# Performance work log

Measured on AMD Instinct MI355X. Metric: run time of the kernel, lower is better.

The kernel has to match this reference:

```python
import jax, jax.numpy as jnp
import numpy as np

D_MODEL = 512
NUM_HEADS = 8
DEPTH = D_MODEL // NUM_HEADS
PROJ_DIM = 256
SEQ_LEN = 4096
BATCH = 8


def _glorot(key, shape):
    fan_in, fan_out = shape[-2], shape[-1]
    limit = np.sqrt(6.0 / (fan_in + fan_out))
    return jax.random.uniform(key, shape, jnp.float32, -limit, limit)


def setup_inputs() -> dict:
    key = jax.random.key(0)
    ks = jax.random.split(key, 8)
    x = jax.random.normal(ks[0], (BATCH, SEQ_LEN, D_MODEL), jnp.float32)
    wq = _glorot(ks[1], (D_MODEL, D_MODEL))
    wk = _glorot(ks[2], (D_MODEL, D_MODEL))
    wv = _glorot(ks[3], (D_MODEL, D_MODEL))
    E = _glorot(ks[4], (NUM_HEADS, SEQ_LEN, PROJ_DIM))
    F = _glorot(ks[5], (NUM_HEADS, SEQ_LEN, PROJ_DIM))
    w_out = _glorot(ks[6], (D_MODEL, D_MODEL))
    b_out = jnp.zeros((D_MODEL,), jnp.float32)
    return {"x": x, "wq": wq, "wk": wk, "wv": wv, "E": E, "F": F,
            "w_out": w_out, "b_out": b_out}


def reference(x, wq, wk, wv, E, F, w_out, b_out):
    b, n, _ = x.shape
    # QKV projections + split heads -> [b, h, n, d]
    def split_heads(t):
        return t.reshape(b, n, NUM_HEADS, DEPTH).transpose(0, 2, 1, 3)
    q = split_heads(x @ wq)
    k = split_heads(x @ wk)
    v = split_heads(x @ wv)
    # Linformer low-rank projection of K/V along sequence: [b,h,r,d]
    k_proj = jnp.einsum('bhnd,hnr->bhrd', k, E)
    v_proj = jnp.einsum('bhnd,hnr->bhrd', v, F)
    scale = 1.0 / jnp.sqrt(jnp.asarray(DEPTH, jnp.float32))
    scores = jnp.einsum('bhnd,bhrd->bhnr', q, k_proj) * scale  # [b,h,n,r]
    attn = jax.nn.softmax(scores, axis=-1)
    out = jnp.einsum('bhnr,bhrd->bhnd', attn, v_proj)
    out = out.transpose(0, 2, 1, 3).reshape(b, n, D_MODEL)
    return out @ w_out + b_out
```

## Files before the change

kernel.cpp:

```cpp
#include <hip/hip_runtime.h>

typedef unsigned short u16;
typedef unsigned int   u32;
typedef __bf16 bf16x8 __attribute__((ext_vector_type(8)));
typedef float  f32x4  __attribute__((ext_vector_type(4)));
typedef u16    u16x4  __attribute__((ext_vector_type(4)));

#define DEV __device__ __forceinline__

DEV u16 f2bf(float f) {
    u32 u = __builtin_bit_cast(u32, f);
    u = (u + 0x7fffu + ((u >> 16) & 1u)) >> 16;
    return (u16)u;
}

DEV void gload16(const void* g, void* l) {
    __builtin_amdgcn_global_load_lds((const __attribute__((address_space(1))) u32*)g,
                                     (__attribute__((address_space(3))) u32*)l, 16, 0, 0);
}

DEV void vmw(int n) {
    switch (n) {
        case 0:  asm volatile("s_waitcnt vmcnt(0)" ::: "memory"); break;
        case 4:  asm volatile("s_waitcnt vmcnt(4)" ::: "memory"); break;
        case 8:  asm volatile("s_waitcnt vmcnt(8)" ::: "memory"); break;
        default: asm volatile("s_waitcnt vmcnt(10)" ::: "memory"); break;
    }
}

__global__ __launch_bounds__(256) void k_prep(const float* __restrict__ x,
                                              const float* __restrict__ wq, const float* __restrict__ wk,
                                              const float* __restrict__ wv, const float* __restrict__ wo,
                                              const float* __restrict__ E, const float* __restrict__ F,
                                              u16* __restrict__ xb, u16* __restrict__ wcatT, u16* __restrict__ woT,
                                              u16* __restrict__ Et, u16* __restrict__ Ft) {
    __shared__ u16 tile[64][65];
    const int t = threadIdx.x;
    const int bid = blockIdx.x;
    if (bid < 16384) {
        int i = (bid * 256 + t) * 4;
        float4 v = *(const float4*)(x + i);
        u16x4 o;
        o[0] = f2bf(v.x); o[1] = f2bf(v.y); o[2] = f2bf(v.z); o[3] = f2bf(v.w);
        *(u16x4*)(xb + i) = o;
    } else if (bid < 20480) {
        const int b2 = bid - 16384;
        const int rt = b2 & 3, ntl = (b2 >> 2) & 63, h = (b2 >> 8) & 7, which = b2 >> 11;
        const float* src = (which ? F : E) + (size_t)h * 4096 * 256;
        u16* dst = (which ? Ft : Et) + (size_t)h * 256 * 4096;
        const int n0 = ntl * 64, r0 = rt * 64;
#pragma unroll
        for (int it = 0; it < 16; ++it) {
            const int idx = t + it * 256;
            const int nl = idx >> 6, rl = idx & 63;
            tile[nl][rl] = f2bf(src[(size_t)(n0 + nl) * 256 + r0 + rl]);
        }
        __syncthreads();
#pragma unroll
        for (int it = 0; it < 16; ++it) {
            const int idx = t + it * 256;
            const int rl = idx >> 6, nl = idx & 63;
            dst[(size_t)(r0 + rl) * 4096 + n0 + nl] = tile[nl][rl];
        }
    } else {
        const int b2 = bid - 20480;
        const int mi = b2 >> 6, tix = b2 & 63;
        const int jt = tix & 7, kt = tix >> 3;
        const float* w = (mi == 0) ? wq : (mi == 1) ? wk : (mi == 2) ? wv : wo;
        u16* dst = (mi < 3) ? (wcatT + mi * 262144) : woT;
#pragma unroll
        for (int it = 0; it < 16; ++it) {
            const int idx = t + it * 256;
            const int kl = idx >> 6, jl = idx & 63;
            tile[kl][jl] = f2bf(w[(kt * 64 + kl) * 512 + jt * 64 + jl]);
        }
        __syncthreads();
#pragma unroll
        for (int it = 0; it < 16; ++it) {
            const int idx = t + it * 256;
            const int jl = idx >> 6, kl = idx & 63;
            dst[(size_t)(jt * 64 + jl) * 512 + kt * 64 + kl] = tile[kl][jl];
        }
    }
}

template <int MODE>
__global__ __launch_bounds__(512, 2) void k_gemm8(const u16* __restrict__ A, const u16* __restrict__ Bm,
                                                  u16* __restrict__ Qo, u16* __restrict__ Kt, u16* __restrict__ Vt,
                                                  float* __restrict__ Of, const float* __restrict__ bias,
                                                  int M, int N, int K) {
    __shared__ __attribute__((aligned(16))) char smem[131072];
    const int tid = threadIdx.x;
    const int lane = tid & 63, w = tid >> 6;
    const int wr = w >> 2, wcn = w & 3;
    const int g = lane >> 4, l16 = lane & 15;
    const int nbm = M >> 8;
    const int bnc = N >> 8;
    const int bandw = nbm >> 3;
    const int bid = (int)blockIdx.x;
    const int xcd = bid & 7, loc = bid >> 3;
    const int bm = xcd * bandw + loc / bnc;
    const int bn = loc % bnc;
    const int m0 = bm << 8, n0 = bn << 8;
    const int NT = K >> 6;

    auto stage_h = [&](int h) {
        const int ktile = h >> 2, ty = h & 3;
        const int kh = ty >> 1;
        const int isB = ty & 1;
        const int slot = (ktile * 2 + kh) & 3;
        const u16* src = isB ? Bm : A;
        const int r0 = isB ? n0 : m0;
        char* base = smem + isB * 65536 + slot * 16384;
#pragma unroll
        for (int j = 0; j < 2; ++j) {
            const int off = j * 8192 + tid * 16;
            const int row = off >> 6, c = (off >> 4) & 3;
            const int sc = c ^ ((row >> 1) & 3);
            gload16(src + (size_t)(r0 + row) * K + ktile * 64 + kh * 32 + sc * 8, base + off);
        }
    };

    for (int h = 0; h < 6; ++h) stage_h(h);
    vmw(8);
    __builtin_amdgcn_sched_barrier(0);
    __builtin_amdgcn_s_barrier();

    f32x4 acc[8][4] = {};
    bf16x8 av[8];
    for (int kt = 0; kt < NT; ++kt) {
#pragma unroll
        for (int s = 0; s < 4; ++s) {
            const int kh = s >> 1, nh = s & 1;
            const int slot = (kt * 2 + kh) & 3;
            char* abase = smem + slot * 16384;
            char* bbase = smem + 65536 + slot * 16384;
            if (nh == 0) {
#pragma unroll
                for (int m = 0; m < 8; ++m) {
                    const int row = wr * 128 + m * 16 + l16;
                    const int c = g ^ ((row >> 1) & 3);
                    av[m] = *(const bf16x8*)(abase + row * 64 + c * 16);
                }
            }
            bf16x8 bv[2];
#pragma unroll
            for (int n = 0; n < 2; ++n) {
                const int col = wcn * 64 + nh * 32 + n * 16 + l16;
                const int c = g ^ ((col >> 1) & 3);
                bv[n] = *(const bf16x8*)(bbase + col * 64 + c * 16);
            }
            const int hst = kt * 4 + s + 6;
            if (hst < NT * 4) stage_h(hst);
            __builtin_amdgcn_s_setprio(1);
#pragma unroll
            for (int m = 0; m < 8; ++m)
#pragma unroll
                for (int n = 0; n < 2; ++n)
                    acc[m][nh * 2 + n] = __builtin_amdgcn_mfma_f32_16x16x32_bf16(av[m], bv[n], acc[m][nh * 2 + n], 0, 0, 0);
            __builtin_amdgcn_s_setprio(0);
            const bool last = (kt == NT - 1) && (s == 3);
            if (!last) {
                int n;
                if (s == 0)      n = (kt < NT - 1) ? 10 : 4;
                else if (s == 1) n = (kt < NT - 1) ? 8 : 0;
                else if (s == 2) n = (kt < NT - 2) ? 10 : ((kt == NT - 2) ? 8 : 0);
                else             n = (kt < NT - 2) ? 8 : 4;
                vmw(n);
                __builtin_amdgcn_sched_barrier(0);
                __builtin_amdgcn_s_barrier();
            }
        }
    }

    if (MODE == 0) {
        if (n0 < 512) {
#pragma unroll
            for (int m = 0; m < 8; ++m)
#pragma unroll
                for (int jn = 0; jn < 4; ++jn) {
                    const int col = n0 + wcn * 64 + jn * 16 + l16;
#pragma unroll
                    for (int i = 0; i < 4; ++i) {
                        const int row = m0 + wr * 128 + m * 16 + g * 4 + i;
                        Qo[(size_t)row * 512 + col] = f2bf(acc[m][jn][i]);
                    }
                }
        } else {
            u16* dst = (n0 < 1024) ? Kt : Vt;
#pragma unroll
            for (int m = 0; m < 8; ++m)
#pragma unroll
                for (int jn = 0; jn < 4; ++jn) {
                    const int col = (n0 + wcn * 64 + jn * 16 + l16) & 511;
                    const int h = col >> 6, d = col & 63;
                    const int rowb = m0 + wr * 128 + m * 16 + g * 4;
                    const int b = rowb >> 12, nn = rowb & 4095;
                    u16x4 pk;
#pragma unroll
                    for (int i = 0; i < 4; ++i) pk[i] = f2bf(acc[m][jn][i]);
                    *(u16x4*)(dst + ((size_t)((b * 8 + h) * 64 + d)) * 4096 + nn) = pk;
                }
        }
    } else {
#pragma unroll
        for (int m = 0; m < 8; ++m)
#pragma unroll
            for (int jn = 0; jn < 4; ++jn) {
                const int col = n0 + wcn * 64 + jn * 16 + l16;
                const float bb = bias[col];
#pragma unroll
                for (int i = 0; i < 4; ++i) {
                    const int row = m0 + wr * 128 + m * 16 + g * 4 + i;
                    Of[(size_t)row * N + col] = acc[m][jn][i] + bb;
                }
            }
    }
}

__global__ __launch_bounds__(256) void k_proj(const u16* __restrict__ Et, const u16* __restrict__ Ft,
                                              const u16* __restrict__ Kt, const u16* __restrict__ Vt,
                                              float* __restrict__ pbuf) {
    __shared__ __attribute__((aligned(16))) char smem[24576];
    const int tid = threadIdx.x;
    const int lane = tid & 63, wid = tid >> 6;
    const int wr = wid >> 1, wc = wid & 1;
    const int g = lane >> 4, l16 = lane & 15;
    const int bid = blockIdx.x;
    const int sp = bid >> 8, rest = bid & 255;
    const int mt = rest & 1, which = (rest >> 1) & 1, bh = rest >> 2;
    const int h = bh & 7;
    const u16* Ap = (which ? Ft : Et) + (size_t)h * 256 * 4096 + (size_t)mt * 128 * 4096;
    const u16* Bp = (which ? Vt : Kt) + (size_t)bh * 64 * 4096;

    f32x4 acc[4][2] = {};

    const int kbeg = sp * 1024;
    for (int k0 = kbeg; k0 < kbeg + 1024; k0 += 64) {
#pragma unroll
        for (int c = 0; c < 4; ++c) {
            const int off = c * 4096 + tid * 16;
            const int row = off >> 7;
            const int sc = ((off >> 4) & 7) ^ (row & 7);
            gload16(Ap + (size_t)row * 4096 + (k0 + sc * 8), smem + off);
            if (c < 2)
                gload16(Bp + (size_t)row * 4096 + (k0 + sc * 8), smem + 16384 + off);
        }
        __syncthreads();
#pragma unroll
        for (int kk = 0; kk < 64; kk += 32) {
            bf16x8 av[4], bv[2];
#pragma unroll
            for (int m = 0; m < 4; ++m) {
                const int r = wr * 64 + m * 16 + l16;
                av[m] = *(const bf16x8*)(smem + r * 128 + ((kk * 2 + g * 16) ^ ((r & 7) << 4)));
            }
#pragma unroll
            for (int n = 0; n < 2; ++n) {
                const int r = wc * 32 + n * 16 + l16;
                bv[n] = *(const bf16x8*)(smem + 16384 + r * 128 + ((kk * 2 + g * 16) ^ ((r & 7) << 4)));
            }
            __builtin_amdgcn_s_setprio(1);
#pragma unroll
            for (int m = 0; m < 4; ++m)
#pragma unroll
                for (int n = 0; n < 2; ++n)
                    acc[m][n] = __builtin_amdgcn_mfma_f32_16x16x32_bf16(av[m], bv[n], acc[m][n], 0, 0, 0);
            __builtin_amdgcn_s_setprio(0);
        }
        __syncthreads();
    }

    float* pb = pbuf + ((size_t)(sp * 2 + which) * 64 + bh) * 16384;
    if (which == 0) {
#pragma unroll
        for (int m = 0; m < 4; ++m)
#pragma unroll
            for (int n = 0; n < 2; ++n) {
                const int d = wc * 32 + n * 16 + l16;
#pragma unroll
                for (int i = 0; i < 4; ++i) {
                    const int rg = mt * 128 + wr * 64 + m * 16 + g * 4 + i;
                    pb[rg * 64 + d] = acc[m][n][i];
                }
            }
    } else {
#pragma unroll
        for (int m = 0; m < 4; ++m)
#pragma unroll
            for (int n = 0; n < 2; ++n) {
                const int d = wc * 32 + n * 16 + l16;
                const int r4 = mt * 128 + wr * 64 + m * 16 + g * 4;
                *(f32x4*)(pb + d * 256 + r4) = acc[m][n];
            }
    }
}

__global__ __launch_bounds__(256) void k_preduce(const float* __restrict__ pbuf, u16* __restrict__ outkv) {
    const int o = ((int)blockIdx.x * 256 + (int)threadIdx.x) * 4;
    f32x4 s = *(const f32x4*)(pbuf + o);
    s += *(const f32x4*)(pbuf + 2097152 + o);
    s += *(const f32x4*)(pbuf + 4194304 + o);
    s += *(const f32x4*)(pbuf + 6291456 + o);
    u16x4 r;
#pragma unroll
    for (int i = 0; i < 4; ++i) r[i] = f2bf(s[i]);
    *(u16x4*)(outkv + o) = r;
}

__global__ __launch_bounds__(256) void k_flash(const u16* __restrict__ Q, const u16* __restrict__ kp,
                                               const u16* __restrict__ vpT, u16* __restrict__ ctx) {
    __shared__ __attribute__((aligned(16))) char smem[65536];
    const int tid = threadIdx.x;
    const int lane = tid & 63, w = tid >> 6;
    const int g = lane >> 4, l16 = lane & 15;
    const int bid = blockIdx.x;
    const int nt = bid & 63, bh = bid >> 6;
    const int b = bh >> 3, h = bh & 7;
    const int n0 = nt * 64;

#pragma unroll
    for (int c = 0; c < 8; ++c) {
        const int off = c * 4096 + tid * 16;
        {
            const int row = off >> 7;
            const int sc = ((off >> 4) & 7) ^ (row & 7);
            gload16(kp + (size_t)bh * 16384 + row * 64 + sc * 8, smem + off);
        }
        {
            const int row = off >> 9;
            const int sc = ((off >> 4) & 31) ^ (row & 7);
            gload16(vpT + (size_t)bh * 16384 + row * 256 + sc * 8, smem + 32768 + off);
        }
    }
    const size_t qbase = (size_t)(b * 4096 + n0 + w * 16 + l16) * 512 + h * 64 + g * 8;
    bf16x8 qf0 = *(const bf16x8*)(Q + qbase);
    bf16x8 qf1 = *(const bf16x8*)(Q + qbase + 32);
    __syncthreads();

    f32x4 s[16];
    __builtin_amdgcn_s_setprio(1);
#pragma unroll
    for (int rt = 0; rt < 16; ++rt) {
        const int r = rt * 16 + l16;
        const int sw = (r & 7) << 4;
        bf16x8 kv0 = *(const bf16x8*)(smem + r * 128 + ((g * 16) ^ sw));
        bf16x8 kv1 = *(const bf16x8*)(smem + r * 128 + ((64 + g * 16) ^ sw));
        f32x4 z = {0.f, 0.f, 0.f, 0.f};
        z = __builtin_amdgcn_mfma_f32_16x16x32_bf16(qf0, kv0, z, 0, 0, 0);
        z = __builtin_amdgcn_mfma_f32_16x16x32_bf16(qf1, kv1, z, 0, 0, 0);
        s[rt] = z;
    }
    __builtin_amdgcn_s_setprio(0);

    float mx[4] = {-1e30f, -1e30f, -1e30f, -1e30f};
#pragma unroll
    for (int rt = 0; rt < 16; ++rt)
#pragma unroll
        for (int i = 0; i < 4; ++i) {
            s[rt][i] *= 0.125f;
            mx[i] = fmaxf(mx[i], s[rt][i]);
        }
#pragma unroll
    for (int i = 0; i < 4; ++i) {
        mx[i] = fmaxf(mx[i], __shfl_xor(mx[i], 1));
        mx[i] = fmaxf(mx[i], __shfl_xor(mx[i], 2));
        mx[i] = fmaxf(mx[i], __shfl_xor(mx[i], 4));
        mx[i] = fmaxf(mx[i], __shfl_xor(mx[i], 8));
    }
    float sm[4] = {0.f, 0.f, 0.f, 0.f};
#pragma unroll
    for (int rt = 0; rt < 16; ++rt)
#pragma unroll
        for (int i = 0; i < 4; ++i) {
            float e = __expf(s[rt][i] - mx[i]);
            s[rt][i] = e;
            sm[i] += e;
        }
#pragma unroll
    for (int i = 0; i < 4; ++i) {
        sm[i] += __shfl_xor(sm[i], 1);
        sm[i] += __shfl_xor(sm[i], 2);
        sm[i] += __shfl_xor(sm[i], 4);
        sm[i] += __shfl_xor(sm[i], 8);
    }

    __syncthreads();

#pragma unroll
    for (int rt = 0; rt < 16; ++rt)
#pragma unroll
        for (int i = 0; i < 4; ++i) {
            const int nrow = g * 4 + i;
            const int byte = w * 8192 + nrow * 512 + ((rt * 32 + l16 * 2) ^ ((nrow & 7) << 4));
            *(u16*)(smem + byte) = f2bf(s[rt][i]);
        }
    bf16x8 af[8];
#pragma unroll
    for (int ks = 0; ks < 8; ++ks) {
        const int byte = w * 8192 + l16 * 512 + ((ks * 64 + g * 16) ^ ((l16 & 7) << 4));
        af[ks] = *(const bf16x8*)(smem + byte);
    }
    f32x4 o[4] = {};
    __builtin_amdgcn_s_setprio(1);
#pragma unroll
    for (int dt = 0; dt < 4; ++dt)
#pragma unroll
        for (int ks = 0; ks < 8; ++ks) {
            const int row = dt * 16 + l16;
            const int byte = 32768 + row * 512 + ((ks * 64 + g * 16) ^ ((row & 7) << 4));
            bf16x8 bv = *(const bf16x8*)(smem + byte);
            o[dt] = __builtin_amdgcn_mfma_f32_16x16x32_bf16(af[ks], bv, o[dt], 0, 0, 0);
        }
    __builtin_amdgcn_s_setprio(0);
    float rinv[4];
#pragma unroll
    for (int i = 0; i < 4; ++i) rinv[i] = 1.0f / sm[i];
#pragma unroll
    for (int dt = 0; dt < 4; ++dt)
#pragma unroll
        for (int i = 0; i < 4; ++i) {
            const int row = b * 4096 + n0 + w * 16 + g * 4 + i;
            const int col = h * 64 + dt * 16 + l16;
            ctx[(size_t)row * 512 + col] = f2bf(o[dt][i] * rinv[i]);
        }
}


extern "C" void kernel_launch(void* const* d_in, const int* in_sizes, int n_in,
                              void* d_out, int out_size, void* d_ws, size_t ws_size,
                              hipStream_t stream) {
    const float* x  = (const float*)d_in[0];
    const float* wq = (const float*)d_in[1];
    const float* wk = (const float*)d_in[2];
    const float* wv = (const float*)d_in[3];
    const float* E  = (const float*)d_in[4];
    const float* F  = (const float*)d_in[5];
    const float* wo = (const float*)d_in[6];
    const float* bo = (const float*)d_in[7];
    float* out = (float*)d_out;
    u16* ws = (u16*)d_ws;

    u16* xb    = ws;
    u16* Qm    = ws + 16777216;
    u16* Kt    = ws + 33554432;
    u16* Vt    = ws + 50331648;
    u16* Et    = ws + 67108864;
    u16* Ft    = ws + 75497472;
    u16* wcatT = ws + 83886080;
    u16* woT   = ws + 84672512;
    u16* kpB   = ws + 84934656;
    u16* vpT   = ws + 85983232;
    float* pbuf = (float*)xb;
    u16* ctx   = xb;

    k_prep<<<20736, 256, 0, stream>>>(x, wq, wk, wv, wo, E, F, xb, wcatT, woT, Et, Ft);
    k_gemm8<0><<<768, 512, 0, stream>>>(xb, wcatT, Qm, Kt, Vt, nullptr, nullptr, 32768, 1536, 512);
    k_proj<<<1024, 256, 0, stream>>>(Et, Ft, Kt, Vt, pbuf);
    k_preduce<<<2048, 256, 0, stream>>>(pbuf, kpB);
    k_flash<<<4096, 256, 0, stream>>>(Qm, kpB, vpT, ctx);
    k_gemm8<1><<<256, 512, 0, stream>>>(ctx, woT, nullptr, nullptr, nullptr, out, bo, 32768, 512, 512);
}
```

Baseline: 368.2 us.

## Vectorize prep transposes, simplify GEMM pipeline, and reuse K/V tiles across query blocks

The prep kernel now reads float4 and writes u16x4 when transposing weights and E/F, with padded tiles. The GEMM main loop stages A and B half-k tiles together and runs a simpler loop of 32 MFMAs per step with its own waitcnt schedule. The attention kernel now runs 512 threads per block and loops over four 128-row query chunks, so each block loads the projected K/V tile into shared memory once for 512 query rows instead of 64. The trade-off is far fewer blocks, 128KB of LDS per block, and serial per-chunk work inside each block.

```diff
diff --git a/kernel.cpp b/kernel.cpp
--- a/kernel.cpp
+++ b/kernel.cpp
@@ -23,8 +23,7 @@
     switch (n) {
         case 0:  asm volatile("s_waitcnt vmcnt(0)" ::: "memory"); break;
         case 4:  asm volatile("s_waitcnt vmcnt(4)" ::: "memory"); break;
-        case 8:  asm volatile("s_waitcnt vmcnt(8)" ::: "memory"); break;
-        default: asm volatile("s_waitcnt vmcnt(10)" ::: "memory"); break;
+        default: asm volatile("s_waitcnt vmcnt(8)" ::: "memory"); break;
     }
 }
 
@@ -34,7 +33,7 @@
                                               const float* __restrict__ E, const float* __restrict__ F,
                                               u16* __restrict__ xb, u16* __restrict__ wcatT, u16* __restrict__ woT,
                                               u16* __restrict__ Et, u16* __restrict__ Ft) {
-    __shared__ u16 tile[64][65];
+    __shared__ u16 tile[64][68];
     const int t = threadIdx.x;
     const int bid = blockIdx.x;
     if (bid < 16384) {
@@ -50,17 +49,22 @@
         u16* dst = (which ? Ft : Et) + (size_t)h * 256 * 4096;
         const int n0 = ntl * 64, r0 = rt * 64;
 #pragma unroll
-        for (int it = 0; it < 16; ++it) {
+        for (int it = 0; it < 4; ++it) {
             const int idx = t + it * 256;
-            const int nl = idx >> 6, rl = idx & 63;
-            tile[nl][rl] = f2bf(src[(size_t)(n0 + nl) * 256 + r0 + rl]);
+            const int nl = idx >> 4, rq = (idx & 15) * 4;
+            float4 v = *(const float4*)(src + (size_t)(n0 + nl) * 256 + r0 + rq);
+            tile[rq + 0][nl] = f2bf(v.x);
+            tile[rq + 1][nl] = f2bf(v.y);
+            tile[rq + 2][nl] = f2bf(v.z);
+            tile[rq + 3][nl] = f2bf(v.w);
         }
         __syncthreads();
 #pragma unroll
-        for (int it = 0; it < 16; ++it) {
+        for (int it = 0; it < 4; ++it) {
             const int idx = t + it * 256;
-            const int rl = idx >> 6, nl = idx & 63;
-            dst[(size_t)(r0 + rl) * 4096 + n0 + nl] = tile[nl][rl];
+            const int rl = idx >> 4, nq = (idx & 15) * 4;
+            u16x4 vv = *(const u16x4*)&tile[rl][nq];
+            *(u16x4*)(dst + (size_t)(r0 + rl) * 4096 + n0 + nq) = vv;
         }
     } else {
         const int b2 = bid - 20480;
@@ -69,17 +73,22 @@
         const float* w = (mi == 0) ? wq : (mi == 1) ? wk : (mi == 2) ? wv : wo;
         u16* dst = (mi < 3) ? (wcatT + mi * 262144) : woT;
 #pragma unroll
-        for (int it = 0; it < 16; ++it) {
+        for (int it = 0; it < 4; ++it) {
             const int idx = t + it * 256;
-            const int kl = idx >> 6, jl = idx & 63;
-            tile[kl][jl] = f2bf(w[(kt * 64 + kl) * 512 + jt * 64 + jl]);
+            const int kl = idx >> 4, jq = (idx & 15) * 4;
+            float4 v = *(const float4*)(w + (size_t)(kt * 64 + kl) * 512 + jt * 64 + jq);
+            tile[jq + 0][kl] = f2bf(v.x);
+            tile[jq + 1][kl] = f2bf(v.y);
+            tile[jq + 2][kl] = f2bf(v.z);
+            tile[jq + 3][kl] = f2bf(v.w);
         }
         __syncthreads();
 #pragma unroll
-        for (int it = 0; it < 16; ++it) {
+        for (int it = 0; it < 4; ++it) {
             const int idx = t + it * 256;
-            const int jl = idx >> 6, kl = idx & 63;
-            dst[(size_t)(jt * 64 + jl) * 512 + kt * 64 + kl] = tile[kl][jl];
+            const int jl = idx >> 4, kq = (idx & 15) * 4;
+            u16x4 vv = *(const u16x4*)&tile[jl][kq];
+            *(u16x4*)(dst + (size_t)(jt * 64 + jl) * 512 + kt * 64 + kq) = vv;
         }
     }
 }
@@ -102,74 +111,61 @@
     const int bm = xcd * bandw + loc / bnc;
     const int bn = loc % bnc;
     const int m0 = bm << 8, n0 = bn << 8;
-    const int NT = K >> 6;
-
-    auto stage_h = [&](int h) {
-        const int ktile = h >> 2, ty = h & 3;
-        const int kh = ty >> 1;
-        const int isB = ty & 1;
-        const int slot = (ktile * 2 + kh) & 3;
-        const u16* src = isB ? Bm : A;
-        const int r0 = isB ? n0 : m0;
-        char* base = smem + isB * 65536 + slot * 16384;
-#pragma unroll
-        for (int j = 0; j < 2; ++j) {
-            const int off = j * 8192 + tid * 16;
-            const int row = off >> 6, c = (off >> 4) & 3;
-            const int sc = c ^ ((row >> 1) & 3);
-            gload16(src + (size_t)(r0 + row) * K + ktile * 64 + kh * 32 + sc * 8, base + off);
+    const int NP = K >> 5;
+
+    auto stage_pair = [&](int P) {
+        const int kt = P >> 1, kh = P & 1;
+        const int slot = P & 3;
+#pragma unroll
+        for (int isB = 0; isB < 2; ++isB) {
+            const u16* src = isB ? Bm : A;
+            const int r0 = isB ? n0 : m0;
+            char* base = smem + isB * 65536 + slot * 16384;
+#pragma unroll
+            for (int j = 0; j < 2; ++j) {
+                const int off = j * 8192 + tid * 16;
+                const int row = off >> 6, c = (off >> 4) & 3;
+                const int sc = c ^ ((row >> 1) & 3);
+                gload16(src + (size_t)(r0 + row) * K + kt * 64 + kh * 32 + sc * 8, base + off);
+            }
         }
     };
 
-    for (int h = 0; h < 6; ++h) stage_h(h);
+    stage_pair(0); stage_pair(1); stage_pair(2);
     vmw(8);
     __builtin_amdgcn_sched_barrier(0);
     __builtin_amdgcn_s_barrier();
 
     f32x4 acc[8][4] = {};
-    bf16x8 av[8];
-    for (int kt = 0; kt < NT; ++kt) {
-#pragma unroll
-        for (int s = 0; s < 4; ++s) {
-            const int kh = s >> 1, nh = s & 1;
-            const int slot = (kt * 2 + kh) & 3;
-            char* abase = smem + slot * 16384;
-            char* bbase = smem + 65536 + slot * 16384;
-            if (nh == 0) {
-#pragma unroll
-                for (int m = 0; m < 8; ++m) {
-                    const int row = wr * 128 + m * 16 + l16;
-                    const int c = g ^ ((row >> 1) & 3);
-                    av[m] = *(const bf16x8*)(abase + row * 64 + c * 16);
-                }
-            }
-            bf16x8 bv[2];
-#pragma unroll
-            for (int n = 0; n < 2; ++n) {
-                const int col = wcn * 64 + nh * 32 + n * 16 + l16;
-                const int c = g ^ ((col >> 1) & 3);
-                bv[n] = *(const bf16x8*)(bbase + col * 64 + c * 16);
-            }
-            const int hst = kt * 4 + s + 6;
-            if (hst < NT * 4) stage_h(hst);
-            __builtin_amdgcn_s_setprio(1);
-#pragma unroll
-            for (int m = 0; m < 8; ++m)
-#pragma unroll
-                for (int n = 0; n < 2; ++n)
-                    acc[m][nh * 2 + n] = __builtin_amdgcn_mfma_f32_16x16x32_bf16(av[m], bv[n], acc[m][nh * 2 + n], 0, 0, 0);
-            __builtin_amdgcn_s_setprio(0);
-            const bool last = (kt == NT - 1) && (s == 3);
-            if (!last) {
-                int n;
-                if (s == 0)      n = (kt < NT - 1) ? 10 : 4;
-                else if (s == 1) n = (kt < NT - 1) ? 8 : 0;
-                else if (s == 2) n = (kt < NT - 2) ? 10 : ((kt == NT - 2) ? 8 : 0);
-                else             n = (kt < NT - 2) ? 8 : 4;
-                vmw(n);
-                __builtin_amdgcn_sched_barrier(0);
-                __builtin_amdgcn_s_barrier();
-            }
+    for (int P = 0; P < NP; ++P) {
+        const int slot = P & 3;
+        char* abase = smem + slot * 16384;
+        char* bbase = smem + 65536 + slot * 16384;
+        bf16x8 av[8], bv[4];
+#pragma unroll
+        for (int m = 0; m < 8; ++m) {
+            const int row = wr * 128 + m * 16 + l16;
+            const int c = g ^ ((row >> 1) & 3);
+            av[m] = *(const bf16x8*)(abase + row * 64 + c * 16);
+        }
+#pragma unroll
+        for (int n = 0; n < 4; ++n) {
+            const int col = wcn * 64 + n * 16 + l16;
+            const int c = g ^ ((col >> 1) & 3);
+            bv[n] = *(const bf16x8*)(bbase + col * 64 + c * 16);
+        }
+        if (P + 3 < NP) stage_pair(P + 3);
+        __builtin_amdgcn_s_setprio(1);
+#pragma unroll
+        for (int m = 0; m < 8; ++m)
+#pragma unroll
+            for (int n = 0; n < 4; ++n)
+                acc[m][n] = __builtin_amdgcn_mfma_f32_16x16x32_bf16(av[m], bv[n], acc[m][n], 0, 0, 0);
+        __builtin_amdgcn_s_setprio(0);
+        if (P < NP - 1) {
+            vmw(P < NP - 3 ? 8 : (P == NP - 3 ? 4 : 0));
+            __builtin_amdgcn_sched_barrier(0);
+            __builtin_amdgcn_s_barrier();
         }
     }
 
@@ -308,20 +304,20 @@
     *(u16x4*)(outkv + o) = r;
 }
 
-__global__ __launch_bounds__(256) void k_flash(const u16* __restrict__ Q, const u16* __restrict__ kp,
+__global__ __launch_bounds__(512) void k_flash(const u16* __restrict__ Q, const u16* __restrict__ kp,
                                                const u16* __restrict__ vpT, u16* __restrict__ ctx) {
-    __shared__ __attribute__((aligned(16))) char smem[65536];
+    __shared__ __attribute__((aligned(16))) char smem[131072];
     const int tid = threadIdx.x;
     const int lane = tid & 63, w = tid >> 6;
     const int g = lane >> 4, l16 = lane & 15;
     const int bid = blockIdx.x;
-    const int nt = bid & 63, bh = bid >> 6;
+    const int seg = bid & 7, bh = bid >> 3;
     const int b = bh >> 3, h = bh & 7;
-    const int n0 = nt * 64;
-
-#pragma unroll
-    for (int c = 0; c < 8; ++c) {
-        const int off = c * 4096 + tid * 16;
+    const int n0 = seg * 512;
+
+#pragma unroll
+    for (int c = 0; c < 4; ++c) {
+        const int off = c * 8192 + tid * 16;
         {
             const int row = off >> 7;
             const int sc = ((off >> 4) & 7) ^ (row & 7);
@@ -333,97 +329,104 @@
             gload16(vpT + (size_t)bh * 16384 + row * 256 + sc * 8, smem + 32768 + off);
         }
     }
-    const size_t qbase = (size_t)(b * 4096 + n0 + w * 16 + l16) * 512 + h * 64 + g * 8;
-    bf16x8 qf0 = *(const bf16x8*)(Q + qbase);
-    bf16x8 qf1 = *(const bf16x8*)(Q + qbase + 32);
+    const size_t qrow0 = (size_t)(b * 4096 + n0 + w * 16 + l16) * 512 + h * 64 + g * 8;
+    bf16x8 qf0 = *(const bf16x8*)(Q + qrow0);
+    bf16x8 qf1 = *(const bf16x8*)(Q + qrow0 + 32);
     __syncthreads();
 
-    f32x4 s[16];
-    __builtin_amdgcn_s_setprio(1);
-#pragma unroll
-    for (int rt = 0; rt < 16; ++rt) {
-        const int r = rt * 16 + l16;
-        const int sw = (r & 7) << 4;
-        bf16x8 kv0 = *(const bf16x8*)(smem + r * 128 + ((g * 16) ^ sw));
-        bf16x8 kv1 = *(const bf16x8*)(smem + r * 128 + ((64 + g * 16) ^ sw));
-        f32x4 z = {0.f, 0.f, 0.f, 0.f};
-        z = __builtin_amdgcn_mfma_f32_16x16x32_bf16(qf0, kv0, z, 0, 0, 0);
-        z = __builtin_amdgcn_mfma_f32_16x16x32_bf16(qf1, kv1, z, 0, 0, 0);
-        s[rt] = z;
-    }
-    __builtin_amdgcn_s_setprio(0);
-
-    float mx[4] = {-1e30f, -1e30f, -1e30f, -1e30f};
-#pragma unroll
-    for (int rt = 0; rt < 16; ++rt)
+    const int pbase = 65536 + w * 8192;
+    for (int qp = 0; qp < 4; ++qp) {
+        f32x4 s[16];
+        __builtin_amdgcn_s_setprio(1);
+#pragma unroll
+        for (int rt = 0; rt < 16; ++rt) {
+            const int r = rt * 16 + l16;
+            const int sw = (r & 7) << 4;
+            bf16x8 kv0 = *(const bf16x8*)(smem + r * 128 + ((g * 16) ^ sw));
+            bf16x8 kv1 = *(const bf16x8*)(smem + r * 128 + ((64 + g * 16) ^ sw));
+            f32x4 z = {0.f, 0.f, 0.f, 0.f};
+            z = __builtin_amdgcn_mfma_f32_16x16x32_bf16(qf0, kv0, z, 0, 0, 0);
+            z = __builtin_amdgcn_mfma_f32_16x16x32_bf16(qf1, kv1, z, 0, 0, 0);
+            s[rt] = z;
+        }
+        __builtin_amdgcn_s_setprio(0);
+
+        if (qp < 3) {
+            const size_t qn = qrow0 + (size_t)(qp + 1) * 128 * 512;
+            qf0 = *(const bf16x8*)(Q + qn);
+            qf1 = *(const bf16x8*)(Q + qn + 32);
+        }
+
+        float mx[4] = {-1e30f, -1e30f, -1e30f, -1e30f};
+#pragma unroll
+        for (int rt = 0; rt < 16; ++rt)
+#pragma unroll
+            for (int i = 0; i < 4; ++i) {
+                s[rt][i] *= 0.125f;
+                mx[i] = fmaxf(mx[i], s[rt][i]);
+            }
 #pragma unroll
         for (int i = 0; i < 4; ++i) {
-            s[rt][i] *= 0.125f;
-            mx[i] = fmaxf(mx[i], s[rt][i]);
-        }
-#pragma unroll
-    for (int i = 0; i < 4; ++i) {
-        mx[i] = fmaxf(mx[i], __shfl_xor(mx[i], 1));
-        mx[i] = fmaxf(mx[i], __shfl_xor(mx[i], 2));
-        mx[i] = fmaxf(mx[i], __shfl_xor(mx[i], 4));
-        mx[i] = fmaxf(mx[i], __shfl_xor(mx[i], 8));
-    }
-    float sm[4] = {0.f, 0.f, 0.f, 0.f};
-#pragma unroll
-    for (int rt = 0; rt < 16; ++rt)
+            mx[i] = fmaxf(mx[i], __shfl_xor(mx[i], 1));
+            mx[i] = fmaxf(mx[i], __shfl_xor(mx[i], 2));
+            mx[i] = fmaxf(mx[i], __shfl_xor(mx[i], 4));
+            mx[i] = fmaxf(mx[i], __shfl_xor(mx[i], 8));
+        }
+        float sm[4] = {0.f, 0.f, 0.f, 0.f};
+#pragma unroll
+        for (int rt = 0; rt < 16; ++rt)
+#pragma unroll
+            for (int i = 0; i < 4; ++i) {
+                float e = __expf(s[rt][i] - mx[i]);
+                s[rt][i] = e;
+                sm[i] += e;
+            }
 #pragma unroll
         for (int i = 0; i < 4; ++i) {
-            float e = __expf(s[rt][i] - mx[i]);
-            s[rt][i] = e;
-            sm[i] += e;
-        }
-#pragma unroll
-    for (int i = 0; i < 4; ++i) {
-        sm[i] += __shfl_xor(sm[i], 1);
-        sm[i] += __shfl_xor(sm[i], 2);
-        sm[i] += __shfl_xor(sm[i], 4);
-        sm[i] += __shfl_xor(sm[i], 8);
-    }
-
-    __syncthreads();
-
-#pragma unroll
-    for (int rt = 0; rt < 16; ++rt)
-#pragma unroll
-        for (int i = 0; i < 4; ++i) {
-            const int nrow = g * 4 + i;
-            const int byte = w * 8192 + nrow * 512 + ((rt * 32 + l16 * 2) ^ ((nrow & 7) << 4));
-            *(u16*)(smem + byte) = f2bf(s[rt][i]);
-        }
-    bf16x8 af[8];
-#pragma unroll
-    for (int ks = 0; ks < 8; ++ks) {
-        const int byte = w * 8192 + l16 * 512 + ((ks * 64 + g * 16) ^ ((l16 & 7) << 4));
-        af[ks] = *(const bf16x8*)(smem + byte);
-    }
-    f32x4 o[4] = {};
-    __builtin_amdgcn_s_setprio(1);
-#pragma unroll
-    for (int dt = 0; dt < 4; ++dt)
+            sm[i] += __shfl_xor(sm[i], 1);
+            sm[i] += __shfl_xor(sm[i], 2);
+            sm[i] += __shfl_xor(sm[i], 4);
+            sm[i] += __shfl_xor(sm[i], 8);
+        }
+
+#pragma unroll
+        for (int rt = 0; rt < 16; ++rt)
+#pragma unroll
+            for (int i = 0; i < 4; ++i) {
+                const int nrow = g * 4 + i;
+                const int byte = pbase + nrow * 512 + ((rt * 32 + l16 * 2) ^ ((nrow & 7) << 4));
+                *(u16*)(smem + byte) = f2bf(s[rt][i]);
+            }
+        bf16x8 af[8];
 #pragma unroll
         for (int ks = 0; ks < 8; ++ks) {
-            const int row = dt * 16 + l16;
-            const int byte = 32768 + row * 512 + ((ks * 64 + g * 16) ^ ((row & 7) << 4));
-            bf16x8 bv = *(const bf16x8*)(smem + byte);
-            o[dt] = __builtin_amdgcn_mfma_f32_16x16x32_bf16(af[ks], bv, o[dt], 0, 0, 0);
-        }
-    __builtin_amdgcn_s_setprio(0);
-    float rinv[4];
-#pragma unroll
-    for (int i = 0; i < 4; ++i) rinv[i] = 1.0f / sm[i];
-#pragma unroll
-    for (int dt = 0; dt < 4; ++dt)
-#pragma unroll
-        for (int i = 0; i < 4; ++i) {
-            const int row = b * 4096 + n0 + w * 16 + g * 4 + i;
-            const int col = h * 64 + dt * 16 + l16;
-            ctx[(size_t)row * 512 + col] = f2bf(o[dt][i] * rinv[i]);
-        }
+            const int byte = pbase + l16 * 512 + ((ks * 64 + g * 16) ^ ((l16 & 7) << 4));
+            af[ks] = *(const bf16x8*)(smem + byte);
+        }
+        f32x4 o[4] = {};
+        __builtin_amdgcn_s_setprio(1);
+#pragma unroll
+        for (int dt = 0; dt < 4; ++dt)
+#pragma unroll
+            for (int ks = 0; ks < 8; ++ks) {
+                const int row = dt * 16 + l16;
+                const int byte = 32768 + row * 512 + ((ks * 64 + g * 16) ^ ((row & 7) << 4));
+                bf16x8 bv = *(const bf16x8*)(smem + byte);
+                o[dt] = __builtin_amdgcn_mfma_f32_16x16x32_bf16(af[ks], bv, o[dt], 0, 0, 0);
+            }
+        __builtin_amdgcn_s_setprio(0);
+        float rinv[4];
+#pragma unroll
+        for (int i = 0; i < 4; ++i) rinv[i] = 1.0f / sm[i];
+#pragma unroll
+        for (int dt = 0; dt < 4; ++dt)
+#pragma unroll
+            for (int i = 0; i < 4; ++i) {
+                const int row = b * 4096 + n0 + qp * 128 + w * 16 + g * 4 + i;
+                const int col = h * 64 + dt * 16 + l16;
+                ctx[(size_t)row * 512 + col] = f2bf(o[dt][i] * rinv[i]);
+            }
+    }
 }
 
 
@@ -458,6 +461,6 @@
     k_gemm8<0><<<768, 512, 0, stream>>>(xb, wcatT, Qm, Kt, Vt, nullptr, nullptr, 32768, 1536, 512);
     k_proj<<<1024, 256, 0, stream>>>(Et, Ft, Kt, Vt, pbuf);
     k_preduce<<<2048, 256, 0, stream>>>(pbuf, kpB);
-    k_flash<<<4096, 256, 0, stream>>>(Qm, kpB, vpT, ctx);
+    k_flash<<<512, 512, 0, stream>>>(Qm, kpB, vpT, ctx);
     k_gemm8<1><<<256, 512, 0, stream>>>(ctx, woT, nullptr, nullptr, nullptr, out, bo, 32768, 512, 512);
 }
```

Result: no change. 375.6 us (+2.0%).
